# Optimization experiments

Hardware: AMD Instinct MI355X
Metric: run time of the kernel (lower is better)

## Reference

```python
import jax, jax.numpy as jnp
import numpy as np

B, T, C, H = 8, 2048, 768, 64  # batch, seq, n_embed, head_size

def setup_inputs() -> dict:
    key = jax.random.key(0)
    kx, kq, kk, kv = jax.random.split(key, 4)
    x = jax.random.normal(kx, (B, T, C), dtype=jnp.float32)
    Wq = jax.random.normal(kq, (C, H), dtype=jnp.float32) * (C ** -0.5)
    Wk = jax.random.normal(kk, (C, H), dtype=jnp.float32) * (C ** -0.5)
    Wv = jax.random.normal(kv, (C, H), dtype=jnp.float32) * (C ** -0.5)
    return {"x": x, "Wq": Wq, "Wk": Wk, "Wv": Wv}

def reference(x, Wq, Wk, Wv):
    # projections (bias-free linears)
    q = jnp.einsum('btc,ch->bth', x, Wq)
    k = jnp.einsum('btc,ch->bth', x, Wk)
    v = jnp.einsum('btc,ch->bth', x, Wv)
    scale = k.shape[-1] ** -0.5
    wei = jnp.einsum('bth,bsh->bts', q, k) * scale  # [B, T, T]
    Tq = x.shape[1]
    causal = jnp.tril(jnp.ones((Tq, Tq), dtype=bool))
    wei = jnp.where(causal, wei, -jnp.inf)
    wei = jax.nn.softmax(wei, axis=-1)
    # dropout p=0.0 -> identity
    out = jnp.einsum('bts,bsh->bth', wei, v)
    return out
```

## Files before the change

### kernel.cpp

```cpp
#include <hip/hip_runtime.h>


typedef __bf16 bf16x8 __attribute__((ext_vector_type(8)));
typedef float  f32x4  __attribute__((ext_vector_type(4)));
typedef unsigned int u32;

union ABu {
    bf16x8 v;
    uint4  u;
    unsigned short us[8];
};

__device__ __forceinline__ unsigned short f2bf(float f) {
    union { __bf16 h; unsigned short s; } c;
    c.h = (__bf16)f;
    return c.s;
}
__device__ __forceinline__ float bf2f(unsigned short s) {
    union { unsigned int u; float f; } c; c.u = ((unsigned int)s) << 16;
    return c.f;
}

__device__ __forceinline__ void gld16(void* lds, const void* g) {
    __builtin_amdgcn_global_load_lds(
        (const u32 __attribute__((address_space(1)))*)g,
        (u32 __attribute__((address_space(3)))*)lds, 16, 0, 0);
}

__global__ __launch_bounds__(256)
void wt_kernel(const float* __restrict__ Wq, const float* __restrict__ Wk,
               const float* __restrict__ Wv, unsigned short* __restrict__ wF) {
    const int j   = blockIdx.x / 6;
    const int kgg = blockIdx.x % 6;
    const int t = threadIdx.x;
    const int kg = kgg * 4 + (t >> 6);
    const int lane = t & 63, quad = lane >> 4, l16 = lane & 15;
    const int m = j >> 2, nb = (j & 3) * 16;
    const float* W = (m == 0) ? Wq : (m == 1) ? Wk : Wv;
    ABu o;
#pragma unroll
    for (int i = 0; i < 8; ++i)
        o.us[i] = f2bf(W[(kg * 32 + quad * 8 + i) * 64 + nb + l16]);
    *(uint4*)(wF + ((size_t)(j * 24 + kg) * 64 + lane) * 8) = o.u;
}

__global__ __launch_bounds__(512, 4)
void qkv_kernel(const float* __restrict__ x, const unsigned short* __restrict__ wF,
                unsigned short* __restrict__ qF, unsigned short* __restrict__ kF,
                unsigned short* __restrict__ vF) {
    __shared__ float          xs[2][32][68];
    __shared__ unsigned short wsW[2][24][64][8];
    __shared__ unsigned short Cst[2][12][16][17];
    const int tid  = threadIdx.x;
    const int lane = tid & 63, w = tid >> 6;
    const int l16  = lane & 15, quad = lane >> 4;
    const int mh   = w & 1, nh = w >> 1;
    const int m0   = blockIdx.x * 32;
    const int b    = m0 >> 11;

    f32x4 acc[3];
#pragma unroll
    for (int j = 0; j < 3; ++j) acc[j] = (f32x4){0.f, 0.f, 0.f, 0.f};

    const int xrow = tid >> 4, xc16 = tid & 15;

#pragma unroll
    for (int i = 0; i < 3; ++i) {
        const int c = w * 3 + i, j = c >> 1, kg2 = c & 1;
        gld16((char*)wsW[0] + (size_t)c * 1024 + lane * 16,
              (const char*)wF + ((size_t)(j * 24 + kg2) * 64 + lane) * 16);
    }
    *(float4*)&xs[0][xrow][xc16 * 4] =
        *(const float4*)&x[(size_t)(m0 + xrow) * 768 + xc16 * 4];
    __syncthreads();

    for (int kk = 0; kk < 12; ++kk) {
        const int cur = kk & 1, nxt = cur ^ 1;
        float4 xn;
        if (kk + 1 < 12) {
#pragma unroll
            for (int i = 0; i < 3; ++i) {
                const int c = w * 3 + i, j = c >> 1, kg2 = c & 1;
                gld16((char*)wsW[nxt] + (size_t)c * 1024 + lane * 16,
                      (const char*)wF + ((size_t)(j * 24 + (kk + 1) * 2 + kg2) * 64 + lane) * 16);
            }
            xn = *(const float4*)&x[(size_t)(m0 + xrow) * 768 + (kk + 1) * 64 + xc16 * 4];
        }

#pragma unroll
        for (int kg2 = 0; kg2 < 2; ++kg2) {
            const float* xr = &xs[cur][mh * 16 + l16][kg2 * 32 + quad * 8];
            float4 f0 = *(const float4*)xr;
            float4 f1 = *(const float4*)(xr + 4);
            ABu af;
            af.us[0] = f2bf(f0.x); af.us[1] = f2bf(f0.y);
            af.us[2] = f2bf(f0.z); af.us[3] = f2bf(f0.w);
            af.us[4] = f2bf(f1.x); af.us[5] = f2bf(f1.y);
            af.us[6] = f2bf(f1.z); af.us[7] = f2bf(f1.w);
#pragma unroll
            for (int jl = 0; jl < 3; ++jl) {
                const int j = nh * 3 + jl;
                ABu bf;
                bf.u = *(const uint4*)((char*)wsW[cur] + (size_t)(j * 2 + kg2) * 1024 + lane * 16);
                acc[jl] = __builtin_amdgcn_mfma_f32_16x16x32_bf16(af.v, bf.v, acc[jl], 0, 0, 0);
            }
        }

        if (kk + 1 < 12)
            *(float4*)&xs[nxt][xrow][xc16 * 4] = xn;
        __syncthreads();
    }

#pragma unroll
    for (int jl = 0; jl < 3; ++jl)
#pragma unroll
        for (int r = 0; r < 4; ++r)
            Cst[mh][nh * 3 + jl][quad * 4 + r][l16] = f2bf(acc[jl][r]);
    __syncthreads();

    const int g = tid >> 6, el = tid & 63;
    const int eq = el >> 4, e16 = el & 15;
    if (g < 4) {
        const int mhh = g >> 1, kg = g & 1;
        ABu oq, ok;
#pragma unroll
        for (int i = 0; i < 8; ++i) {
            const int h = kg * 32 + eq * 8 + i;
            oq.us[i] = Cst[mhh][h >> 4][e16][h & 15];
            ok.us[i] = Cst[mhh][4 + (h >> 4)][e16][h & 15];
        }
        const size_t tt = (size_t)b * 128 + ((m0 & 2047) >> 4) + mhh;
        *(uint4*)(qF + ((tt * 2 + kg) * 64 + el) * 8) = oq.u;
        *(uint4*)(kF + ((tt * 2 + kg) * 64 + el) * 8) = ok.u;
    } else {
        const int nt = g & 3;
        const int sv = (m0 & 2047) >> 6, kg = (m0 >> 5) & 1;
        ABu ov;
#pragma unroll
        for (int i = 0; i < 8; ++i) {
            const int loc = eq * 8 + i;
            ov.us[i] = Cst[loc >> 4][8 + nt][loc & 15][e16];
        }
        *(uint4*)(vF + ((((size_t)(b * 32 + sv) * 4 + nt) * 2 + kg) * 64 + el) * 8) = ov.u;
    }
}

__global__ __launch_bounds__(256, 4)
void attn_kernel(const unsigned short* __restrict__ qF,
                 const unsigned short* __restrict__ kF,
                 const unsigned short* __restrict__ vF,
                 unsigned short* __restrict__ opart, float* __restrict__ lpart) {
    __shared__ unsigned short PT[4][64][20];
    const int tid  = threadIdx.x;
    const int lane = tid & 63, w = tid >> 6;
    const int l16  = lane & 15, quad = lane >> 4;
    const int idx  = blockIdx.x;
    const int b    = idx >> 7;
    const int rem  = idx & 127;
    const int jj   = rem >> 2, quarter = rem & 3;
    const int qs   = (jj & 1) ? (31 - (jj >> 1)) : (jj >> 1);
    const int tt   = qs * 4 + w;
    const int tq0  = tt * 16;
    const float SC = 0.125f * 1.44269504089f;
    const float MB = 16.0f  * 1.44269504089f;

    ABu aq[2];
#pragma unroll
    for (int kg = 0; kg < 2; ++kg)
        aq[kg].u = *(const uint4*)(qF + ((((size_t)b * 128 + tt) * 2 + kg) * 64 + lane) * 8);

    f32x4 acc[4];
#pragma unroll
    for (int nt = 0; nt < 4; ++nt) acc[nt] = (f32x4){0.f, 0.f, 0.f, 0.f};
    float lrow[4] = {0.f, 0.f, 0.f, 0.f};

    for (int st = quarter; st <= qs; st += 4) {
        const int s0 = st * 64;
        const unsigned short* kbase = kF + (size_t)(b * 128 + st * 4) * 1024;
        const unsigned short* vbase = vF + (size_t)(b * 32 + st) * 4096;
        ABu kf[8];
#pragma unroll
        for (int c = 0; c < 8; ++c)
            kf[c].u = *(const uint4*)(kbase + (size_t)c * 512 + lane * 8);
        float p[4][4];
#pragma unroll
        for (int nt = 0; nt < 4; ++nt) {
            f32x4 s = (f32x4){0.f, 0.f, 0.f, 0.f};
            s = __builtin_amdgcn_mfma_f32_16x16x32_bf16(aq[0].v, kf[nt * 2 + 0].v, s, 0, 0, 0);
            s = __builtin_amdgcn_mfma_f32_16x16x32_bf16(aq[1].v, kf[nt * 2 + 1].v, s, 0, 0, 0);
            const int sg = s0 + nt * 16 + l16;
#pragma unroll
            for (int r = 0; r < 4; ++r) {
                float pv = __builtin_amdgcn_exp2f(__builtin_fmaf(s[r], SC, -MB));
                pv = (sg > tq0 + quad * 4 + r) ? 0.f : pv;
                p[nt][r] = pv;
                lrow[r] += pv;
            }
        }
        ABu vf[8];
#pragma unroll
        for (int c = 0; c < 8; ++c)
            vf[c].u = *(const uint4*)(vbase + (size_t)c * 512 + lane * 8);
#pragma unroll
        for (int nt = 0; nt < 4; ++nt) {
            ushort4 pw;
            pw.x = f2bf(p[nt][0]); pw.y = f2bf(p[nt][1]);
            pw.z = f2bf(p[nt][2]); pw.w = f2bf(p[nt][3]);
            *(ushort4*)&PT[w][nt * 16 + l16][quad * 4] = pw;
        }
        ABu ap[2];
#pragma unroll
        for (int ks = 0; ks < 2; ++ks)
#pragma unroll
            for (int j = 0; j < 8; ++j)
                ap[ks].us[j] = PT[w][ks * 32 + quad * 8 + j][l16];
#pragma unroll
        for (int nt = 0; nt < 4; ++nt) {
            acc[nt] = __builtin_amdgcn_mfma_f32_16x16x32_bf16(ap[0].v, vf[nt * 2 + 0].v, acc[nt], 0, 0, 0);
            acc[nt] = __builtin_amdgcn_mfma_f32_16x16x32_bf16(ap[1].v, vf[nt * 2 + 1].v, acc[nt], 0, 0, 0);
        }
    }

#pragma unroll
    for (int off = 1; off <= 8; off <<= 1)
#pragma unroll
        for (int r = 0; r < 4; ++r)
            lrow[r] += __shfl_xor(lrow[r], off);

    unsigned short* obase = opart + ((size_t)(quarter * 8 + b) * 2048 + tq0) * 64;
#pragma unroll
    for (int nt = 0; nt < 4; ++nt)
#pragma unroll
        for (int r = 0; r < 4; ++r)
            obase[(size_t)(quad * 4 + r) * 64 + nt * 16 + l16] = f2bf(acc[nt][r]);
    if (l16 == 0) {
#pragma unroll
        for (int r = 0; r < 4; ++r)
            lpart[(size_t)(quarter * 8 + b) * 2048 + tq0 + quad * 4 + r] = lrow[r];
    }
}

__global__ __launch_bounds__(256)
void finalize_kernel(const unsigned short* __restrict__ opart,
                     const float* __restrict__ lpart, float* __restrict__ out) {
    const int idx = blockIdx.x * 256 + threadIdx.x;
    const int row = idx >> 4;
    float4 v = (float4){0.f, 0.f, 0.f, 0.f};
    float  l = 0.f;
#pragma unroll
    for (int q = 0; q < 4; ++q) {
        ushort4 u = ((const ushort4*)opart)[(size_t)q * 262144 + idx];
        v.x += bf2f(u.x); v.y += bf2f(u.y); v.z += bf2f(u.z); v.w += bf2f(u.w);
        l += lpart[(size_t)q * 16384 + row];
    }
    const float li = 1.f / l;
    v.x *= li; v.y *= li; v.z *= li; v.w *= li;
    ((float4*)out)[idx] = v;
}

extern "C" void kernel_launch(void* const* d_in, const int* in_sizes, int n_in,
                              void* d_out, int out_size, void* d_ws, size_t ws_size,
                              hipStream_t stream) {
    const float* x  = (const float*)d_in[0];
    const float* Wq = (const float*)d_in[1];
    const float* Wk = (const float*)d_in[2];
    const float* Wv = (const float*)d_in[3];
    float* out = (float*)d_out;

    char* ws = (char*)d_ws;
    unsigned short* wF    = (unsigned short*)ws;
    unsigned short* qF    = (unsigned short*)(ws + (512 << 10));
    unsigned short* kF    = (unsigned short*)(ws + (512 << 10) + (2 << 20));
    unsigned short* vF    = (unsigned short*)(ws + (512 << 10) + (4 << 20));
    unsigned short* opart = (unsigned short*)(ws + (512 << 10) + (6 << 20));
    float*          lpart = (float*)(ws + (512 << 10) + (14 << 20));

    wt_kernel<<<72, 256, 0, stream>>>(Wq, Wk, Wv, wF);
    qkv_kernel<<<512, 512, 0, stream>>>(x, wF, qF, kF, vF);
    attn_kernel<<<1024, 256, 0, stream>>>(qF, kF, vF, opart, lpart);
    finalize_kernel<<<1024, 256, 0, stream>>>(opart, lpart, out);
}
```

Before: 126.6 us.

## Transpose QK MFMA and use permlane swaps instead of LDS for P

```diff
diff --git a/kernel.cpp b/kernel.cpp
--- a/kernel.cpp
+++ b/kernel.cpp
@@ -19,6 +19,11 @@
 __device__ __forceinline__ float bf2f(unsigned short s) {
     union { unsigned int u; float f; } c; c.u = ((unsigned int)s) << 16;
     return c.f;
+}
+__device__ __forceinline__ u32 cvtpk_bf16(float lo, float hi) {
+    u32 r;
+    asm("v_cvt_pk_bf16_f32 %0, %1, %2" : "=v"(r) : "v"(lo), "v"(hi));
+    return r;
 }
 
 __device__ __forceinline__ void gld16(void* lds, const void* g) {
@@ -93,10 +98,10 @@
             float4 f0 = *(const float4*)xr;
             float4 f1 = *(const float4*)(xr + 4);
             ABu af;
-            af.us[0] = f2bf(f0.x); af.us[1] = f2bf(f0.y);
-            af.us[2] = f2bf(f0.z); af.us[3] = f2bf(f0.w);
-            af.us[4] = f2bf(f1.x); af.us[5] = f2bf(f1.y);
-            af.us[6] = f2bf(f1.z); af.us[7] = f2bf(f1.w);
+            af.u.x = cvtpk_bf16(f0.x, f0.y);
+            af.u.y = cvtpk_bf16(f0.z, f0.w);
+            af.u.z = cvtpk_bf16(f1.x, f1.y);
+            af.u.w = cvtpk_bf16(f1.z, f1.w);
 #pragma unroll
             for (int jl = 0; jl < 3; ++jl) {
                 const int j = nh * 3 + jl;
@@ -145,12 +150,73 @@
     }
 }
 
+template<bool MASKED>
+__device__ __forceinline__ void attn_tile(
+    const int st, const int b, const int tq0,
+    const int lane, const int l16, const int quad,
+    const ABu& aq0, const ABu& aq1,
+    const unsigned short* __restrict__ kF,
+    const unsigned short* __restrict__ vF,
+    f32x4 acc[4], float& lsum)
+{
+    const float SC = 0.125f * 1.44269504089f;
+    const float MB = 16.0f  * 1.44269504089f;
+    const int s0 = st * 64;
+    const unsigned short* kbase = kF + (size_t)(b * 128 + st * 4) * 1024;
+    const unsigned short* vbase = vF + (size_t)(b * 32 + st) * 4096;
+
+    ABu kf[8];
+#pragma unroll
+    for (int c = 0; c < 8; ++c)
+        kf[c].u = *(const uint4*)(kbase + (size_t)c * 512 + lane * 8);
+
+    float p[4][4];
+#pragma unroll
+    for (int nt = 0; nt < 4; ++nt) {
+        f32x4 s = (f32x4){0.f, 0.f, 0.f, 0.f};
+        s = __builtin_amdgcn_mfma_f32_16x16x32_bf16(kf[nt * 2 + 0].v, aq0.v, s, 0, 0, 0);
+        s = __builtin_amdgcn_mfma_f32_16x16x32_bf16(kf[nt * 2 + 1].v, aq1.v, s, 0, 0, 0);
+#pragma unroll
+        for (int r = 0; r < 4; ++r) {
+            float pv = __builtin_amdgcn_exp2f(__builtin_fmaf(s[r], SC, -MB));
+            if (MASKED)
+                pv = (s0 + nt * 16 + quad * 4 + r > tq0 + l16) ? 0.f : pv;
+            p[nt][r] = pv;
+            lsum += pv;
+        }
+    }
+
+    ABu vf[8];
+#pragma unroll
+    for (int c = 0; c < 8; ++c)
+        vf[c].u = *(const uint4*)(vbase + (size_t)c * 512 + lane * 8);
+
+    ABu af[2];
+#pragma unroll
+    for (int ks = 0; ks < 2; ++ks) {
+        u32 x0 = cvtpk_bf16(p[2 * ks][0], p[2 * ks][1]);
+        u32 x1 = cvtpk_bf16(p[2 * ks][2], p[2 * ks][3]);
+        u32 y0 = cvtpk_bf16(p[2 * ks + 1][0], p[2 * ks + 1][1]);
+        u32 y1 = cvtpk_bf16(p[2 * ks + 1][2], p[2 * ks + 1][3]);
+        asm("v_permlane32_swap_b32 %0, %1" : "+v"(x0), "+v"(y0));
+        asm("v_permlane16_swap_b32 %0, %1" : "+v"(x0), "+v"(y0));
+        asm("v_permlane32_swap_b32 %0, %1" : "+v"(x1), "+v"(y1));
+        asm("v_permlane16_swap_b32 %0, %1" : "+v"(x1), "+v"(y1));
+        af[ks].u = (uint4){x0, x1, y0, y1};
+    }
+
+#pragma unroll
+    for (int nt = 0; nt < 4; ++nt) {
+        acc[nt] = __builtin_amdgcn_mfma_f32_16x16x32_bf16(af[0].v, vf[nt * 2 + 0].v, acc[nt], 0, 0, 0);
+        acc[nt] = __builtin_amdgcn_mfma_f32_16x16x32_bf16(af[1].v, vf[nt * 2 + 1].v, acc[nt], 0, 0, 0);
+    }
+}
+
 __global__ __launch_bounds__(256, 4)
 void attn_kernel(const unsigned short* __restrict__ qF,
                  const unsigned short* __restrict__ kF,
                  const unsigned short* __restrict__ vF,
                  unsigned short* __restrict__ opart, float* __restrict__ lpart) {
-    __shared__ unsigned short PT[4][64][20];
     const int tid  = threadIdx.x;
     const int lane = tid & 63, w = tid >> 6;
     const int l16  = lane & 15, quad = lane >> 4;
@@ -161,71 +227,24 @@
     const int qs   = (jj & 1) ? (31 - (jj >> 1)) : (jj >> 1);
     const int tt   = qs * 4 + w;
     const int tq0  = tt * 16;
-    const float SC = 0.125f * 1.44269504089f;
-    const float MB = 16.0f  * 1.44269504089f;
-
-    ABu aq[2];
-#pragma unroll
-    for (int kg = 0; kg < 2; ++kg)
-        aq[kg].u = *(const uint4*)(qF + ((((size_t)b * 128 + tt) * 2 + kg) * 64 + lane) * 8);
+
+    ABu aq0, aq1;
+    aq0.u = *(const uint4*)(qF + ((((size_t)b * 128 + tt) * 2 + 0) * 64 + lane) * 8);
+    aq1.u = *(const uint4*)(qF + ((((size_t)b * 128 + tt) * 2 + 1) * 64 + lane) * 8);
 
     f32x4 acc[4];
 #pragma unroll
     for (int nt = 0; nt < 4; ++nt) acc[nt] = (f32x4){0.f, 0.f, 0.f, 0.f};
-    float lrow[4] = {0.f, 0.f, 0.f, 0.f};
-
-    for (int st = quarter; st <= qs; st += 4) {
-        const int s0 = st * 64;
-        const unsigned short* kbase = kF + (size_t)(b * 128 + st * 4) * 1024;
-        const unsigned short* vbase = vF + (size_t)(b * 32 + st) * 4096;
-        ABu kf[8];
-#pragma unroll
-        for (int c = 0; c < 8; ++c)
-            kf[c].u = *(const uint4*)(kbase + (size_t)c * 512 + lane * 8);
-        float p[4][4];
-#pragma unroll
-        for (int nt = 0; nt < 4; ++nt) {
-            f32x4 s = (f32x4){0.f, 0.f, 0.f, 0.f};
-            s = __builtin_amdgcn_mfma_f32_16x16x32_bf16(aq[0].v, kf[nt * 2 + 0].v, s, 0, 0, 0);
-            s = __builtin_amdgcn_mfma_f32_16x16x32_bf16(aq[1].v, kf[nt * 2 + 1].v, s, 0, 0, 0);
-            const int sg = s0 + nt * 16 + l16;
-#pragma unroll
-            for (int r = 0; r < 4; ++r) {
-                float pv = __builtin_amdgcn_exp2f(__builtin_fmaf(s[r], SC, -MB));
-                pv = (sg > tq0 + quad * 4 + r) ? 0.f : pv;
-                p[nt][r] = pv;
-                lrow[r] += pv;
-            }
-        }
-        ABu vf[8];
-#pragma unroll
-        for (int c = 0; c < 8; ++c)
-            vf[c].u = *(const uint4*)(vbase + (size_t)c * 512 + lane * 8);
-#pragma unroll
-        for (int nt = 0; nt < 4; ++nt) {
-            ushort4 pw;
-            pw.x = f2bf(p[nt][0]); pw.y = f2bf(p[nt][1]);
-            pw.z = f2bf(p[nt][2]); pw.w = f2bf(p[nt][3]);
-            *(ushort4*)&PT[w][nt * 16 + l16][quad * 4] = pw;
-        }
-        ABu ap[2];
-#pragma unroll
-        for (int ks = 0; ks < 2; ++ks)
-#pragma unroll
-            for (int j = 0; j < 8; ++j)
-                ap[ks].us[j] = PT[w][ks * 32 + quad * 8 + j][l16];
-#pragma unroll
-        for (int nt = 0; nt < 4; ++nt) {
-            acc[nt] = __builtin_amdgcn_mfma_f32_16x16x32_bf16(ap[0].v, vf[nt * 2 + 0].v, acc[nt], 0, 0, 0);
-            acc[nt] = __builtin_amdgcn_mfma_f32_16x16x32_bf16(ap[1].v, vf[nt * 2 + 1].v, acc[nt], 0, 0, 0);
-        }
-    }
-
-#pragma unroll
-    for (int off = 1; off <= 8; off <<= 1)
-#pragma unroll
-        for (int r = 0; r < 4; ++r)
-            lrow[r] += __shfl_xor(lrow[r], off);
+    float lsum = 0.f;
+
+    int st = quarter;
+    for (; st < qs; st += 4)
+        attn_tile<false>(st, b, tq0, lane, l16, quad, aq0, aq1, kF, vF, acc, lsum);
+    if (st == qs)
+        attn_tile<true>(st, b, tq0, lane, l16, quad, aq0, aq1, kF, vF, acc, lsum);
+
+    lsum += __shfl_xor(lsum, 16);
+    lsum += __shfl_xor(lsum, 32);
 
     unsigned short* obase = opart + ((size_t)(quarter * 8 + b) * 2048 + tq0) * 64;
 #pragma unroll
@@ -233,11 +252,8 @@
 #pragma unroll
         for (int r = 0; r < 4; ++r)
             obase[(size_t)(quad * 4 + r) * 64 + nt * 16 + l16] = f2bf(acc[nt][r]);
-    if (l16 == 0) {
-#pragma unroll
-        for (int r = 0; r < 4; ++r)
-            lpart[(size_t)(quarter * 8 + b) * 2048 + tq0 + quad * 4 + r] = lrow[r];
-    }
+    if (lane < 16)
+        lpart[(size_t)(quarter * 8 + b) * 2048 + tq0 + lane] = lsum;
 }
 
 __global__ __launch_bounds__(256)
```

Result: faster. 122.2 us (-3.5%).
